# Performance work log

Hardware: AMD Instinct MI355X
Metric: run time of the kernel (lower is better)

## Reference

```python
import jax, jax.numpy as jnp
import numpy as np
import math

B, S, D, H = 4, 2048, 1024, 16
DH = D // H
NEG = -1e10


def setup_inputs() -> dict:
    key = jax.random.key(0)
    k1, k2, k3 = jax.random.split(key, 3)
    x = jax.random.normal(k1, (B, S, D), dtype=jnp.float32)
    # torch nn.Linear weights have shape (out_features, in_features); y = x @ W.T + b
    w1 = jax.random.normal(k2, (3 * D, D), dtype=jnp.float32) * (1.0 / math.sqrt(D))
    b1 = jnp.zeros((3 * D,), dtype=jnp.float32)
    w2 = jax.random.normal(k3, (D, D), dtype=jnp.float32) * (1.0 / math.sqrt(D))
    b2 = jnp.zeros((D,), dtype=jnp.float32)
    return {"x": x, "w1": w1, "b1": b1, "w2": w2, "b2": b2}


def reference(x, w1, b1, w2, b2):
    b, s, d = x.shape
    h, dh = H, d // H
    qkv = x @ w1.T + b1                                  # [B,S,3D]
    q, k, v = jnp.split(qkv, 3, axis=-1)                 # each [B,S,D]
    def heads(t):
        return t.reshape(b, s, h, dh).transpose(0, 2, 1, 3)  # [B,H,S,dh]
    q, k, v = heads(q), heads(k), heads(v)
    # additive causal mask: (1 - tril) * -1e10, as in the original
    mask = (1.0 - jnp.tril(jnp.ones((s, s), dtype=x.dtype))) * NEG
    scores = jnp.einsum('bhqd,bhkd->bhqk', q, k) / math.sqrt(dh) + mask
    attn = jax.nn.softmax(scores, axis=-1)
    o = jnp.einsum('bhqk,bhkd->bhqd', attn, v)           # [B,H,S,dh]
    o = o.transpose(0, 2, 1, 3).reshape(b, s, d)         # [B,S,D]
    return o @ w2.T + b2
```

## Files before the change

### kernel.cpp

```cpp
#include <hip/hip_runtime.h>
#include <stdint.h>


typedef __bf16 bf16;
typedef __attribute__((ext_vector_type(4))) __bf16 bf16x4;
typedef __attribute__((ext_vector_type(8))) __bf16 bf16x8;
typedef __attribute__((ext_vector_type(4))) float f32x4;
typedef __attribute__((ext_vector_type(16))) float f32x16;

#define MFMA16(a, b, c) __builtin_amdgcn_mfma_f32_16x16x32_bf16((a), (b), (c), 0, 0, 0)
#define MFMA32(a, b, c) __builtin_amdgcn_mfma_f32_32x32x16_bf16((a), (b), (c), 0, 0, 0)

#if __has_builtin(__builtin_amdgcn_exp2f)
#define EXP2F(x) __builtin_amdgcn_exp2f(x)
#else
#define EXP2F(x) exp2f(x)
#endif

#define GLOAD_LDS16(gp, lp)                                                    \
  __builtin_amdgcn_global_load_lds(                                            \
      (__attribute__((address_space(1))) void*)(gp),                           \
      (__attribute__((address_space(3))) void*)(lp), 16, 0, 0)

#define SB   2048
#define D3   3072
#define DD   1024
#define QSCALE 0.18033688011112042f

__global__ __launch_bounds__(256) void cast3_kernel(
    const float* __restrict__ x, const float* __restrict__ w1,
    const float* __restrict__ w2, bf16* __restrict__ xb,
    bf16* __restrict__ w1b, bf16* __restrict__ w2b) {
  const int stride = gridDim.x * blockDim.x;
  const int gid = blockIdx.x * blockDim.x + threadIdx.x;
  auto cvt = [](const float* in, bf16* out, int i) {
    float4 v = ((const float4*)in)[i];
    bf16x4 p;
    p[0] = (bf16)v.x; p[1] = (bf16)v.y; p[2] = (bf16)v.z; p[3] = (bf16)v.w;
    *(bf16x4*)(out + (size_t)i * 4) = p;
  };
  for (int i = gid; i < 2097152; i += stride) cvt(x, xb, i);
  for (int i = gid; i < 786432; i += stride) cvt(w1, w1b, i);
  for (int i = gid; i < 262144; i += stride) cvt(w2, w2b, i);
}

template <int OUTMODE, int WM, int WN, int FM, int FN>
__global__ __launch_bounds__(512, 1) void gemmks_kernel(
    const bf16* __restrict__ A, const bf16* __restrict__ Bw,
    const float* __restrict__ bias, void* __restrict__ Cout,
    bf16* __restrict__ VtOut, int M, int N, int K, int NBn) {
  constexpr int BM = WM * FM * 32, BN = WN * FN * 32;
  constexpr int NRA = BM / 64, NRB = BN / 64;
  __shared__ __attribute__((aligned(16))) bf16 As[2][BM * 64];
  __shared__ __attribute__((aligned(16))) bf16 Bs[2][BN * 64];
  const int tid = threadIdx.x;
  const int w = tid >> 6, l = tid & 63;
  const int lr = l & 31, lh = l >> 5;
  const int wm = w / WN, wn = w % WN;
  const int nwg = gridDim.x;
  const int sw = ((int)blockIdx.x % 8) * (nwg / 8) + (int)blockIdx.x / 8;
  const int bn = sw % NBn, bm = sw / NBn;
  const int m0 = bm * BM, n0 = bn * BN;
  const int NT = K >> 6;

  const int srow = l >> 3;
  const int scol = ((l & 7) ^ srow) << 3;

  auto stage = [&](int buf, int kt) {
#pragma unroll
    for (int j = 0; j < NRA; ++j) {
      const int rb = j * 64 + w * 8 + srow;
      GLOAD_LDS16(A + (size_t)(m0 + rb) * K + kt * 64 + scol,
                  (char*)&As[buf][0] + j * 8192 + w * 1024);
    }
#pragma unroll
    for (int j = 0; j < NRB; ++j) {
      const int rb = j * 64 + w * 8 + srow;
      GLOAD_LDS16(Bw + (size_t)(n0 + rb) * K + kt * 64 + scol,
                  (char*)&Bs[buf][0] + j * 8192 + w * 1024);
    }
  };

  f32x16 acc[FM][FN] = {};

  stage(0, 0);
  __syncthreads();

  for (int T = 0; T < NT; ++T) {
    const int buf = T & 1;
    if (T + 1 < NT) stage(buf ^ 1, T + 1);
#pragma unroll
    for (int ks = 0; ks < 4; ++ks) {
      bf16x8 aF[FM], bF[FN];
#pragma unroll
      for (int ti = 0; ti < FM; ++ti) {
        const int r = wm * (FM * 32) + ti * 32 + lr;
        aF[ti] = *(const bf16x8*)((const char*)&As[buf][0] + r * 128 +
                                  (((ks * 2 + lh) ^ (lr & 7)) << 4));
      }
#pragma unroll
      for (int tj = 0; tj < FN; ++tj) {
        const int r = wn * (FN * 32) + tj * 32 + lr;
        bF[tj] = *(const bf16x8*)((const char*)&Bs[buf][0] + r * 128 +
                                  (((ks * 2 + lh) ^ (lr & 7)) << 4));
      }
      __builtin_amdgcn_s_setprio(1);
#pragma unroll
      for (int ti = 0; ti < FM; ++ti)
#pragma unroll
        for (int tj = 0; tj < FN; ++tj)
          acc[ti][tj] = MFMA32(aF[ti], bF[tj], acc[ti][tj]);
      __builtin_amdgcn_s_setprio(0);
    }
    __syncthreads();
  }

#pragma unroll
  for (int ti = 0; ti < FM; ++ti) {
    const int r0 = m0 + wm * (FM * 32) + ti * 32 + 4 * lh;
#pragma unroll
    for (int tj = 0; tj < FN; ++tj) {
      const int colbase = n0 + wn * (FN * 32) + tj * 32;
      const int col = colbase + lr;
      const float bv = bias[col];
      if (OUTMODE == 1 && colbase >= 2 * DD) {
        bf16* lt = (bf16*)((char*)&As[0][0] + w * 2560);
        asm volatile("s_waitcnt lgkmcnt(0)" ::: "memory");
        __builtin_amdgcn_sched_barrier(0);
#pragma unroll
        for (int e = 0; e < 16; ++e) {
          const int row = (e & 3) + 8 * (e >> 2) + 4 * lh;
          lt[lr * 40 + row] = (bf16)(acc[ti][tj][e] + bv);
        }
        asm volatile("s_waitcnt lgkmcnt(0)" ::: "memory");
        __builtin_amdgcn_sched_barrier(0);
        const int colloc = l >> 1;
        const int hd = colbase + colloc - 2 * DD;
        const int sbase = m0 + wm * (FM * 32) + ti * 32;
        const size_t gb = ((size_t)((sbase >> 11) * 1024 + hd)) * SB +
                          (sbase & 2047) + (l & 1) * 8;
#pragma unroll
        for (int it2 = 0; it2 < 2; ++it2) {
          bf16x8 vv = *(const bf16x8*)&lt[colloc * 40 + it2 * 16 + (l & 1) * 8];
          *(bf16x8*)(VtOut + gb + it2 * 16) = vv;
        }
      } else {
#pragma unroll
        for (int e = 0; e < 16; ++e) {
          const int row = r0 + (e & 3) + 8 * (e >> 2);
          float v = acc[ti][tj][e] + bv;
          if (OUTMODE == 1) {
            if (col < DD) v *= QSCALE;
            ((bf16*)Cout)[(size_t)row * N + col] = (bf16)v;
          } else {
            ((float*)Cout)[(size_t)row * N + col] = v;
          }
        }
      }
    }
  }
}

__global__ __launch_bounds__(256, 2) void attn_kernel(
    const bf16* __restrict__ qkv, const bf16* __restrict__ vT,
    bf16* __restrict__ o) {
  __shared__ __attribute__((aligned(16))) bf16 Kt[2][128 * 64];
  __shared__ __attribute__((aligned(16))) bf16 Vt[2][64 * 128];
  const int tid = threadIdx.x;
  const int w = tid >> 6, l = tid & 63;
  const int c = l & 15, g = l >> 4;
  const int pair = blockIdx.x >> 6, bh = blockIdx.x & 63;
  const int b = bh >> 4, h = bh & 15;
  const int qtA = pair, qtB = 15 - pair;
  const int swz = (c & 7) << 4;

  const bf16* qg = qkv + (size_t)(b * SB) * D3 + h * 64;

  auto stage = [&](int kt, int buf) {
#pragma unroll
    for (int j = 0; j < 4; ++j) {
      const int row = w * 32 + j * 8 + (l >> 3);
      const int cs = ((l & 7) ^ (row & 7)) << 3;
      GLOAD_LDS16(qkv + (size_t)(b * SB + kt * 128 + row) * D3 + DD + h * 64 + cs,
                  (char*)&Kt[buf][0] + w * 4096 + j * 1024);
    }
#pragma unroll
    for (int j = 0; j < 4; ++j) {
      const int row = w * 16 + j * 4 + (l >> 4);
      const int cs = ((l & 15) ^ (row & 7)) << 3;
      GLOAD_LDS16(vT + (size_t)(bh * 64 + row) * SB + kt * 128 + cs,
                  (char*)&Vt[buf][0] + w * 4096 + j * 1024);
    }
  };

  stage(0, 0);

  bf16x8 qfA[2][2], qfB[2][2];
#pragma unroll
  for (int mi = 0; mi < 2; ++mi)
#pragma unroll
    for (int dk = 0; dk < 2; ++dk) {
      qfA[mi][dk] = *(const bf16x8*)(qg + (size_t)(qtA * 128 + w * 32 + mi * 16 + c) * D3 + dk * 32 + g * 8);
      qfB[mi][dk] = *(const bf16x8*)(qg + (size_t)(qtB * 128 + w * 32 + mi * 16 + c) * D3 + dk * 32 + g * 8);
    }

  f32x4 ofA[2][4] = {}, ofB[2][4] = {};
  float mA[2] = {-1e30f, -1e30f}, lA[2] = {0.f, 0.f};
  float mB[2] = {-1e30f, -1e30f}, lB[2] = {0.f, 0.f};
  const f32x4 zero = {0.f, 0.f, 0.f, 0.f};

  auto process = [&](int kt, int qt, int buf, bf16x8 (&qf)[2][2], float (&m)[2],
                     float (&lsum)[2], f32x4 (&of)[2][4]) {
    f32x4 sf[2][8];
    __builtin_amdgcn_s_setprio(1);
#pragma unroll
    for (int f = 0; f < 8; ++f) {
      const char* kr = (const char*)&Kt[buf][0] + (f * 16 + c) * 128;
      bf16x8 kb0 = *(const bf16x8*)(kr + ((g * 16) ^ swz));
      bf16x8 kb1 = *(const bf16x8*)(kr + ((64 + g * 16) ^ swz));
#pragma unroll
      for (int mi = 0; mi < 2; ++mi) {
        f32x4 t = MFMA16(kb0, qf[mi][0], zero);
        sf[mi][f] = MFMA16(kb1, qf[mi][1], t);
      }
    }
    __builtin_amdgcn_s_setprio(0);

    if (kt == qt) {
#pragma unroll
      for (int mi = 0; mi < 2; ++mi) {
        const int qloc = w * 32 + mi * 16 + c;
#pragma unroll
        for (int f = 0; f < 8; ++f)
#pragma unroll
          for (int r = 0; r < 4; ++r)
            if (f * 16 + 4 * g + r > qloc) sf[mi][f][r] = -1e30f;
      }
    }

    bf16x8 pa[2][4];
#pragma unroll
    for (int mi = 0; mi < 2; ++mi) {
      float pm = -1e30f;
#pragma unroll
      for (int f = 0; f < 8; ++f)
#pragma unroll
        for (int r = 0; r < 4; ++r) pm = fmaxf(pm, sf[mi][f][r]);
      pm = fmaxf(pm, __shfl_xor(pm, 16, 64));
      pm = fmaxf(pm, __shfl_xor(pm, 32, 64));
      if (__any(pm > m[mi] + 8.f)) {
        const float mnew = fmaxf(m[mi], pm);
        const float sc = EXP2F(m[mi] - mnew);
        m[mi] = mnew;
        lsum[mi] *= sc;
#pragma unroll
        for (int di = 0; di < 4; ++di) of[mi][di] *= sc;
      }
      float rs = 0.f;
#pragma unroll
      for (int f = 0; f < 8; ++f)
#pragma unroll
        for (int r = 0; r < 4; ++r) {
          const float pv = EXP2F(sf[mi][f][r] - m[mi]);
          sf[mi][f][r] = pv;
          rs += pv;
        }
      rs += __shfl_xor(rs, 16, 64);
      rs += __shfl_xor(rs, 32, 64);
      lsum[mi] += rs;
#pragma unroll
      for (int t = 0; t < 4; ++t)
#pragma unroll
        for (int s = 0; s < 4; ++s) {
          pa[mi][t][s]     = (bf16)sf[mi][2 * t][s];
          pa[mi][t][4 + s] = (bf16)sf[mi][2 * t + 1][s];
        }
    }

    __builtin_amdgcn_s_setprio(1);
#pragma unroll
    for (int di = 0; di < 4; ++di) {
      const char* vrow = (const char*)&Vt[buf][0] + (di * 16 + c) * 256;
#pragma unroll
      for (int t = 0; t < 4; ++t) {
        bf16x4 v1 = *(const bf16x4*)(vrow + ((64 * t + 8 * g) ^ swz));
        bf16x4 v2 = *(const bf16x4*)(vrow + ((64 * t + 32 + 8 * g) ^ swz));
        bf16x8 va;
#pragma unroll
        for (int s = 0; s < 4; ++s) { va[s] = v1[s]; va[4 + s] = v2[s]; }
#pragma unroll
        for (int mi = 0; mi < 2; ++mi)
          of[mi][di] = MFMA16(va, pa[mi][t], of[mi][di]);
      }
    }
    __builtin_amdgcn_s_setprio(0);
  };

  __syncthreads();

  int buf = 0;
  for (int kt = 0; kt <= qtB; ++kt) {
    if (kt < qtB) stage(kt + 1, buf ^ 1);
    if (kt <= qtA) process(kt, qtA, buf, qfA, mA, lA, ofA);
    process(kt, qtB, buf, qfB, mB, lB, ofB);
    __syncthreads();
    buf ^= 1;
  }

  auto store_tile = [&](int qt, float (&lsum)[2], f32x4 (&of)[2][4]) {
#pragma unroll
    for (int mi = 0; mi < 2; ++mi) {
      const float inv = 1.0f / lsum[mi];
      const size_t row = (size_t)(b * SB + qt * 128 + w * 32 + mi * 16 + c);
#pragma unroll
      for (int di = 0; di < 4; ++di) {
        bf16x4 st;
#pragma unroll
        for (int r = 0; r < 4; ++r) st[r] = (bf16)(of[mi][di][r] * inv);
        *(bf16x4*)(o + row * DD + h * 64 + di * 16 + 4 * g) = st;
      }
    }
  };
  store_tile(qtA, lA, ofA);
  store_tile(qtB, lB, ofB);
}

extern "C" void kernel_launch(void* const* d_in, const int* in_sizes, int n_in,
                              void* d_out, int out_size, void* d_ws, size_t ws_size,
                              hipStream_t stream) {
  const float* x  = (const float*)d_in[0];
  const float* w1 = (const float*)d_in[1];
  const float* b1 = (const float*)d_in[2];
  const float* w2 = (const float*)d_in[3];
  const float* b2 = (const float*)d_in[4];
  float* out = (float*)d_out;

  bf16* xb   = (bf16*)d_ws;
  bf16* w1b  = xb   + (size_t)8  * 1024 * 1024;
  bf16* w2b  = w1b  + (size_t)3  * 1024 * 1024;
  bf16* qkvb = w2b  + (size_t)1  * 1024 * 1024;
  bf16* vT   = qkvb + (size_t)8192 * 3072;
  bf16* ob   = vT   + (size_t)8  * 1024 * 1024;

  cast3_kernel<<<2048, 256, 0, stream>>>(x, w1, w2, xb, w1b, w2b);

  gemmks_kernel<1, 2, 4, 4, 3><<<256, 512, 0, stream>>>(xb, w1b, b1, qkvb, vT,
                                                        8192, 3072, 1024, 8);
  attn_kernel<<<512, 256, 0, stream>>>(qkvb, vT, ob);
  gemmks_kernel<0, 4, 2, 2, 2><<<256, 512, 0, stream>>>(ob, w2b, b2, out, nullptr,
                                                        8192, 1024, 1024, 8);
}
```

Measured before the change: 153.7 us.

## Fuse fp32-to-bf16 cast of x into QKV GEMM A-tile staging

```diff
diff --git a/kernel.cpp b/kernel.cpp
--- a/kernel.cpp
+++ b/kernel.cpp
@@ -27,9 +27,8 @@
 #define DD   1024
 #define QSCALE 0.18033688011112042f
 
-__global__ __launch_bounds__(256) void cast3_kernel(
-    const float* __restrict__ x, const float* __restrict__ w1,
-    const float* __restrict__ w2, bf16* __restrict__ xb,
+__global__ __launch_bounds__(256) void cast2_kernel(
+    const float* __restrict__ w1, const float* __restrict__ w2,
     bf16* __restrict__ w1b, bf16* __restrict__ w2b) {
   const int stride = gridDim.x * blockDim.x;
   const int gid = blockIdx.x * blockDim.x + threadIdx.x;
@@ -39,16 +38,16 @@
     p[0] = (bf16)v.x; p[1] = (bf16)v.y; p[2] = (bf16)v.z; p[3] = (bf16)v.w;
     *(bf16x4*)(out + (size_t)i * 4) = p;
   };
-  for (int i = gid; i < 2097152; i += stride) cvt(x, xb, i);
   for (int i = gid; i < 786432; i += stride) cvt(w1, w1b, i);
   for (int i = gid; i < 262144; i += stride) cvt(w2, w2b, i);
 }
 
 template <int OUTMODE, int WM, int WN, int FM, int FN>
 __global__ __launch_bounds__(512, 1) void gemmks_kernel(
-    const bf16* __restrict__ A, const bf16* __restrict__ Bw,
-    const float* __restrict__ bias, void* __restrict__ Cout,
-    bf16* __restrict__ VtOut, int M, int N, int K, int NBn) {
+    const bf16* __restrict__ A, const float* __restrict__ Axf,
+    const bf16* __restrict__ Bw, const float* __restrict__ bias,
+    void* __restrict__ Cout, bf16* __restrict__ VtOut,
+    int M, int N, int K, int NBn) {
   constexpr int BM = WM * FM * 32, BN = WN * FN * 32;
   constexpr int NRA = BM / 64, NRB = BN / 64;
   __shared__ __attribute__((aligned(16))) bf16 As[2][BM * 64];
@@ -66,13 +65,37 @@
   const int srow = l >> 3;
   const int scol = ((l & 7) ^ srow) << 3;
 
-  auto stage = [&](int buf, int kt) {
+  float4 ar[NRA][2];
+
+  auto loadA = [&](int kt) {
+#pragma unroll
+    for (int j = 0; j < NRA; ++j) {
+      const int rb = j * 64 + w * 8 + srow;
+      const float* src = Axf + (size_t)(m0 + rb) * K + kt * 64 + scol;
+      ar[j][0] = *(const float4*)src;
+      ar[j][1] = *(const float4*)(src + 4);
+    }
+  };
+  auto writeA = [&](int buf) {
+#pragma unroll
+    for (int j = 0; j < NRA; ++j) {
+      bf16x8 v;
+      v[0] = (bf16)ar[j][0].x; v[1] = (bf16)ar[j][0].y;
+      v[2] = (bf16)ar[j][0].z; v[3] = (bf16)ar[j][0].w;
+      v[4] = (bf16)ar[j][1].x; v[5] = (bf16)ar[j][1].y;
+      v[6] = (bf16)ar[j][1].z; v[7] = (bf16)ar[j][1].w;
+      *(bf16x8*)((char*)&As[buf][0] + j * 8192 + w * 1024 + l * 16) = v;
+    }
+  };
+  auto stageA_dma = [&](int buf, int kt) {
 #pragma unroll
     for (int j = 0; j < NRA; ++j) {
       const int rb = j * 64 + w * 8 + srow;
       GLOAD_LDS16(A + (size_t)(m0 + rb) * K + kt * 64 + scol,
                   (char*)&As[buf][0] + j * 8192 + w * 1024);
     }
+  };
+  auto stageB = [&](int buf, int kt) {
 #pragma unroll
     for (int j = 0; j < NRB; ++j) {
       const int rb = j * 64 + w * 8 + srow;
@@ -83,12 +106,18 @@
 
   f32x16 acc[FM][FN] = {};
 
-  stage(0, 0);
+  if constexpr (OUTMODE == 1) { loadA(0); writeA(0); }
+  else                        { stageA_dma(0, 0); }
+  stageB(0, 0);
   __syncthreads();
 
   for (int T = 0; T < NT; ++T) {
     const int buf = T & 1;
-    if (T + 1 < NT) stage(buf ^ 1, T + 1);
+    if (T + 1 < NT) {
+      if constexpr (OUTMODE == 1) loadA(T + 1);
+      else                        stageA_dma(buf ^ 1, T + 1);
+      stageB(buf ^ 1, T + 1);
+    }
 #pragma unroll
     for (int ks = 0; ks < 4; ++ks) {
       bf16x8 aF[FM], bF[FN];
@@ -111,6 +140,9 @@
         for (int tj = 0; tj < FN; ++tj)
           acc[ti][tj] = MFMA32(aF[ti], bF[tj], acc[ti][tj]);
       __builtin_amdgcn_s_setprio(0);
+    }
+    if (T + 1 < NT) {
+      if constexpr (OUTMODE == 1) writeA(buf ^ 1);
     }
     __syncthreads();
   }
@@ -342,11 +374,11 @@
   bf16* vT   = qkvb + (size_t)8192 * 3072;
   bf16* ob   = vT   + (size_t)8  * 1024 * 1024;
 
-  cast3_kernel<<<2048, 256, 0, stream>>>(x, w1, w2, xb, w1b, w2b);
-
-  gemmks_kernel<1, 2, 4, 4, 3><<<256, 512, 0, stream>>>(xb, w1b, b1, qkvb, vT,
-                                                        8192, 3072, 1024, 8);
+  cast2_kernel<<<512, 256, 0, stream>>>(w1, w2, w1b, w2b);
+
+  gemmks_kernel<1, 2, 4, 4, 3><<<256, 512, 0, stream>>>(
+      nullptr, x, w1b, b1, qkvb, vT, 8192, 3072, 1024, 8);
   attn_kernel<<<512, 256, 0, stream>>>(qkvb, vT, ob);
-  gemmks_kernel<0, 4, 2, 2, 2><<<256, 512, 0, stream>>>(ob, w2b, b2, out, nullptr,
-                                                        8192, 1024, 1024, 8);
+  gemmks_kernel<0, 4, 2, 2, 2><<<256, 512, 0, stream>>>(
+      ob, nullptr, w2b, b2, out, nullptr, 8192, 1024, 1024, 8);
 }
```

Result: slower. 204.9 us (+33.3%).

## Split attention work across 8 waves with 16 query rows each

Applied to the files above, without the earlier changes.

```diff
diff --git a/kernel.cpp b/kernel.cpp
--- a/kernel.cpp
+++ b/kernel.cpp
@@ -161,7 +161,7 @@
   }
 }
 
-__global__ __launch_bounds__(256, 2) void attn_kernel(
+__global__ __launch_bounds__(512, 4) void attn_kernel(
     const bf16* __restrict__ qkv, const bf16* __restrict__ vT,
     bf16* __restrict__ o) {
   __shared__ __attribute__((aligned(16))) bf16 Kt[2][128 * 64];
@@ -178,104 +178,93 @@
 
   auto stage = [&](int kt, int buf) {
 #pragma unroll
-    for (int j = 0; j < 4; ++j) {
-      const int row = w * 32 + j * 8 + (l >> 3);
+    for (int j = 0; j < 2; ++j) {
+      const int row = w * 16 + j * 8 + (l >> 3);
       const int cs = ((l & 7) ^ (row & 7)) << 3;
       GLOAD_LDS16(qkv + (size_t)(b * SB + kt * 128 + row) * D3 + DD + h * 64 + cs,
-                  (char*)&Kt[buf][0] + w * 4096 + j * 1024);
-    }
-#pragma unroll
-    for (int j = 0; j < 4; ++j) {
-      const int row = w * 16 + j * 4 + (l >> 4);
+                  (char*)&Kt[buf][0] + w * 2048 + j * 1024);
+    }
+#pragma unroll
+    for (int j = 0; j < 2; ++j) {
+      const int row = w * 8 + j * 4 + (l >> 4);
       const int cs = ((l & 15) ^ (row & 7)) << 3;
       GLOAD_LDS16(vT + (size_t)(bh * 64 + row) * SB + kt * 128 + cs,
-                  (char*)&Vt[buf][0] + w * 4096 + j * 1024);
+                  (char*)&Vt[buf][0] + w * 2048 + j * 1024);
     }
   };
 
   stage(0, 0);
 
-  bf16x8 qfA[2][2], qfB[2][2];
-#pragma unroll
-  for (int mi = 0; mi < 2; ++mi)
-#pragma unroll
-    for (int dk = 0; dk < 2; ++dk) {
-      qfA[mi][dk] = *(const bf16x8*)(qg + (size_t)(qtA * 128 + w * 32 + mi * 16 + c) * D3 + dk * 32 + g * 8);
-      qfB[mi][dk] = *(const bf16x8*)(qg + (size_t)(qtB * 128 + w * 32 + mi * 16 + c) * D3 + dk * 32 + g * 8);
-    }
-
-  f32x4 ofA[2][4] = {}, ofB[2][4] = {};
-  float mA[2] = {-1e30f, -1e30f}, lA[2] = {0.f, 0.f};
-  float mB[2] = {-1e30f, -1e30f}, lB[2] = {0.f, 0.f};
+  bf16x8 qfA[2], qfB[2];
+#pragma unroll
+  for (int dk = 0; dk < 2; ++dk) {
+    qfA[dk] = *(const bf16x8*)(qg + (size_t)(qtA * 128 + w * 16 + c) * D3 + dk * 32 + g * 8);
+    qfB[dk] = *(const bf16x8*)(qg + (size_t)(qtB * 128 + w * 16 + c) * D3 + dk * 32 + g * 8);
+  }
+
+  f32x4 ofA[4] = {}, ofB[4] = {};
+  float mA = -1e30f, lA = 0.f, mB = -1e30f, lB = 0.f;
   const f32x4 zero = {0.f, 0.f, 0.f, 0.f};
 
-  auto process = [&](int kt, int qt, int buf, bf16x8 (&qf)[2][2], float (&m)[2],
-                     float (&lsum)[2], f32x4 (&of)[2][4]) {
-    f32x4 sf[2][8];
+  auto process = [&](int kt, int qt, int buf, bf16x8 (&qf)[2], float& m,
+                     float& lsum, f32x4 (&of)[4]) {
+    f32x4 sf[8];
     __builtin_amdgcn_s_setprio(1);
 #pragma unroll
     for (int f = 0; f < 8; ++f) {
       const char* kr = (const char*)&Kt[buf][0] + (f * 16 + c) * 128;
       bf16x8 kb0 = *(const bf16x8*)(kr + ((g * 16) ^ swz));
       bf16x8 kb1 = *(const bf16x8*)(kr + ((64 + g * 16) ^ swz));
-#pragma unroll
-      for (int mi = 0; mi < 2; ++mi) {
-        f32x4 t = MFMA16(kb0, qf[mi][0], zero);
-        sf[mi][f] = MFMA16(kb1, qf[mi][1], t);
-      }
+      f32x4 t = MFMA16(kb0, qf[0], zero);
+      sf[f] = MFMA16(kb1, qf[1], t);
     }
     __builtin_amdgcn_s_setprio(0);
 
     if (kt == qt) {
-#pragma unroll
-      for (int mi = 0; mi < 2; ++mi) {
-        const int qloc = w * 32 + mi * 16 + c;
-#pragma unroll
-        for (int f = 0; f < 8; ++f)
-#pragma unroll
-          for (int r = 0; r < 4; ++r)
-            if (f * 16 + 4 * g + r > qloc) sf[mi][f][r] = -1e30f;
-      }
-    }
-
-    bf16x8 pa[2][4];
-#pragma unroll
-    for (int mi = 0; mi < 2; ++mi) {
-      float pm = -1e30f;
+      const int qloc = w * 16 + c;
 #pragma unroll
       for (int f = 0; f < 8; ++f)
 #pragma unroll
-        for (int r = 0; r < 4; ++r) pm = fmaxf(pm, sf[mi][f][r]);
-      pm = fmaxf(pm, __shfl_xor(pm, 16, 64));
-      pm = fmaxf(pm, __shfl_xor(pm, 32, 64));
-      if (__any(pm > m[mi] + 8.f)) {
-        const float mnew = fmaxf(m[mi], pm);
-        const float sc = EXP2F(m[mi] - mnew);
-        m[mi] = mnew;
-        lsum[mi] *= sc;
-#pragma unroll
-        for (int di = 0; di < 4; ++di) of[mi][di] *= sc;
-      }
-      float rs = 0.f;
-#pragma unroll
-      for (int f = 0; f < 8; ++f)
-#pragma unroll
-        for (int r = 0; r < 4; ++r) {
-          const float pv = EXP2F(sf[mi][f][r] - m[mi]);
-          sf[mi][f][r] = pv;
-          rs += pv;
-        }
-      rs += __shfl_xor(rs, 16, 64);
-      rs += __shfl_xor(rs, 32, 64);
-      lsum[mi] += rs;
-#pragma unroll
-      for (int t = 0; t < 4; ++t)
-#pragma unroll
-        for (int s = 0; s < 4; ++s) {
-          pa[mi][t][s]     = (bf16)sf[mi][2 * t][s];
-          pa[mi][t][4 + s] = (bf16)sf[mi][2 * t + 1][s];
-        }
-    }
+        for (int r = 0; r < 4; ++r)
+          if (f * 16 + 4 * g + r > qloc) sf[f][r] = -1e30f;
+    }
+
+    float pm = -1e30f;
+#pragma unroll
+    for (int f = 0; f < 8; ++f)
+#pragma unroll
+      for (int r = 0; r < 4; ++r) pm = fmaxf(pm, sf[f][r]);
+    pm = fmaxf(pm, __shfl_xor(pm, 16, 64));
+    pm = fmaxf(pm, __shfl_xor(pm, 32, 64));
+    if (__any(pm > m + 8.f)) {
+      const float mnew = fmaxf(m, pm);
+      const float sc = EXP2F(m - mnew);
+      m = mnew;
+      lsum *= sc;
+#pragma unroll
+      for (int di = 0; di < 4; ++di) of[di] *= sc;
+    }
+    float rs = 0.f;
+#pragma unroll
+    for (int f = 0; f < 8; ++f)
+#pragma unroll
+      for (int r = 0; r < 4; ++r) {
+        const float pv = EXP2F(sf[f][r] - m);
+        sf[f][r] = pv;
+        rs += pv;
+      }
+    rs += __shfl_xor(rs, 16, 64);
+    rs += __shfl_xor(rs, 32, 64);
+    lsum += rs;
+
+    bf16x8 pa[4];
+#pragma unroll
+    for (int t = 0; t < 4; ++t)
+#pragma unroll
+      for (int s = 0; s < 4; ++s) {
+        pa[t][s]     = (bf16)sf[2 * t][s];
+        pa[t][4 + s] = (bf16)sf[2 * t + 1][s];
+      }
 
     __builtin_amdgcn_s_setprio(1);
 #pragma unroll
@@ -288,9 +277,7 @@
         bf16x8 va;
 #pragma unroll
         for (int s = 0; s < 4; ++s) { va[s] = v1[s]; va[4 + s] = v2[s]; }
-#pragma unroll
-        for (int mi = 0; mi < 2; ++mi)
-          of[mi][di] = MFMA16(va, pa[mi][t], of[mi][di]);
+        of[di] = MFMA16(va, pa[t], of[di]);
       }
     }
     __builtin_amdgcn_s_setprio(0);
@@ -307,18 +294,15 @@
     buf ^= 1;
   }
 
-  auto store_tile = [&](int qt, float (&lsum)[2], f32x4 (&of)[2][4]) {
-#pragma unroll
-    for (int mi = 0; mi < 2; ++mi) {
-      const float inv = 1.0f / lsum[mi];
-      const size_t row = (size_t)(b * SB + qt * 128 + w * 32 + mi * 16 + c);
-#pragma unroll
-      for (int di = 0; di < 4; ++di) {
-        bf16x4 st;
-#pragma unroll
-        for (int r = 0; r < 4; ++r) st[r] = (bf16)(of[mi][di][r] * inv);
-        *(bf16x4*)(o + row * DD + h * 64 + di * 16 + 4 * g) = st;
-      }
+  auto store_tile = [&](int qt, float lsum, f32x4 (&of)[4]) {
+    const float inv = 1.0f / lsum;
+    const size_t row = (size_t)(b * SB + qt * 128 + w * 16 + c);
+#pragma unroll
+    for (int di = 0; di < 4; ++di) {
+      bf16x4 st;
+#pragma unroll
+      for (int r = 0; r < 4; ++r) st[r] = (bf16)(of[di][r] * inv);
+      *(bf16x4*)(o + row * DD + h * 64 + di * 16 + 4 * g) = st;
     }
   };
   store_tile(qtA, lA, ofA);
@@ -346,7 +330,7 @@
 
   gemmks_kernel<1, 2, 4, 4, 3><<<256, 512, 0, stream>>>(xb, w1b, b1, qkvb, vT,
                                                         8192, 3072, 1024, 8);
-  attn_kernel<<<512, 256, 0, stream>>>(qkvb, vT, ob);
+  attn_kernel<<<512, 512, 0, stream>>>(qkvb, vT, ob);
   gemmks_kernel<0, 4, 2, 2, 2><<<256, 512, 0, stream>>>(ob, w2b, b2, out, nullptr,
                                                         8192, 1024, 1024, 8);
 }
```

Result: slower. 168.9 us (+9.9%).
